# Kernel tuning notes

Measured on AMD Instinct MI355X. Metric: run time of the kernel, lower is better.

## Reference

```python
import jax, jax.numpy as jnp
import numpy as np

RES = 128          # image / k-space resolution
DECIMATION = 4     # acceleration factor
P = RES * RES // DECIMATION  # 4096 trajectory points
B = 8              # batch


def setup_inputs() -> dict:
    key = jax.random.key(0)
    k1, k2 = jax.random.split(key)
    k_space_input = jax.random.normal(k1, (B, 1, RES, RES, 2), dtype=jnp.float32)
    # learnable k-space trajectory in pixel units, range [-RES/2, RES/2]
    trajectory = (jax.random.uniform(k2, (P, 2), dtype=jnp.float32) - 0.5) * RES
    return {"k_space_input": k_space_input, "trajectory": trajectory}


def _grid_sample_points(img, pts_norm):
    """torch.nn.functional.grid_sample (bilinear, zero padding, align_corners=False)
    evaluated at a list of points.
    img: (B, C, H, W); pts_norm: (P, 2) in [-1, 1], [:, 0] -> x (W axis), [:, 1] -> y (H axis).
    Returns (B, C, P)."""
    H, W = img.shape[-2], img.shape[-1]
    x = (pts_norm[:, 0] + 1.0) * (W * 0.5) - 0.5
    y = (pts_norm[:, 1] + 1.0) * (H * 0.5) - 0.5
    x0f = jnp.floor(x)
    y0f = jnp.floor(y)
    wx = x - x0f  # differentiable interpolation weights
    wy = y - y0f
    x0 = x0f.astype(jnp.int32)
    y0 = y0f.astype(jnp.int32)

    def tap(ix, iy, w):
        valid = ((ix >= 0) & (ix < W) & (iy >= 0) & (iy < H)).astype(img.dtype)
        ixc = jnp.clip(ix, 0, W - 1)
        iyc = jnp.clip(iy, 0, H - 1)
        return img[:, :, iyc, ixc] * (w * valid)  # (B, C, P)

    return (tap(x0, y0, (1 - wx) * (1 - wy))
            + tap(x0 + 1, y0, wx * (1 - wy))
            + tap(x0, y0 + 1, (1 - wx) * wy)
            + tap(x0 + 1, y0 + 1, wx * wy))


def _forward(k_space_input, trajectory):
    # (B,1,H,W,2) -> (B,2,H,W): channels = (real, imag)
    ksp = jnp.transpose(k_space_input, (0, 1, 4, 2, 3))[:, 0]
    # bilinear resampling of cartesian k-space at the trajectory points
    pts = trajectory / (RES * 0.5)  # normalize to [-1, 1] as in the torch helper
    sub = _grid_sample_points(ksp, pts)            # (B, 2, P)
    c = sub[:, 0] + 1j * sub[:, 1]                 # complex measurements (B, P)
    # adjoint (type-1) NUFFT back to a centered RES x RES image grid:
    # img[y, x] = (1/RES) * sum_p c[p] * exp(+2*pi*i*(ky_p*y + kx_p*x)/RES)
    xs = jnp.arange(RES, dtype=jnp.float32) - RES * 0.5  # centered grid coords
    phase = (2.0 * jnp.pi / RES)
    Ax = jnp.exp(1j * phase * trajectory[:, 0][:, None] * xs[None, :])  # (P, W)
    Ay = jnp.exp(1j * phase * trajectory[:, 1][:, None] * xs[None, :])  # (P, H)
    tmp = c[:, :, None] * Ay[None, :, :]           # (B, P, H)
    img = jnp.einsum('bph,pw->bhw', tmp, Ax) / RES  # (B, H, W), 1/sqrt(H*W) scale
    out = jnp.stack([img.real, img.imag], axis=-1)[:, None]  # (B, 1, H, W, 2)
    return out


def reference(k_space_input, trajectory):
    return _forward(k_space_input, trajectory)
```

## Files before the change

kernel.cpp:

```cpp
#include <hip/hip_runtime.h>

#define RES    128
#define P_PTS  4096
#define CHUNKS 16
#define PP     256

typedef _Float16 half8  __attribute__((ext_vector_type(8)));
typedef _Float16 half2v __attribute__((ext_vector_type(2)));
typedef float    f32x4  __attribute__((ext_vector_type(4)));

__global__ __launch_bounds__(256) void gemm_kernel(const float* __restrict__ ksp,
                                                   const float* __restrict__ traj,
                                                   half2v* __restrict__ part) {
    __shared__ float2 st[PP];
    __shared__ float2 sc[PP];
    __shared__ __align__(16) _Float16 sA[4096];
    __shared__ __align__(16) _Float16 sB[8192];

    const int chunk = blockIdx.x;
    const int b     = blockIdx.y >> 1;
    const int mh    = blockIdx.y & 1;
    const int tid   = threadIdx.x;
    const int wave  = tid >> 6;
    const int lane  = tid & 63;
    const int l15   = lane & 15;
    const int q     = lane >> 4;

    {
        const int p = chunk * PP + tid;
        const float tx = traj[2 * p], ty = traj[2 * p + 1];
        st[tid] = make_float2(tx, ty);
        const float x = tx + 63.5f, y = ty + 63.5f;
        const float x0f = floorf(x), y0f = floorf(y);
        const float wx = x - x0f, wy = y - y0f;
        const int ix0 = (int)x0f, iy0 = (int)y0f;
        float re = 0.0f, im = 0.0f;
#pragma unroll
        for (int dy = 0; dy < 2; ++dy) {
#pragma unroll
            for (int dx = 0; dx < 2; ++dx) {
                const int ix = ix0 + dx, iy = iy0 + dy;
                const float w = (dx ? wx : 1.0f - wx) * (dy ? wy : 1.0f - wy);
                if (ix >= 0 && ix < RES && iy >= 0 && iy < RES) {
                    const float2 v = *(const float2*)(ksp + ((b * RES + iy) * RES + ix) * 2);
                    re = fmaf(v.x, w, re);
                    im = fmaf(v.y, w, im);
                }
            }
        }
        sc[tid] = make_float2(re * (1.0f / 128.0f), im * (1.0f / 128.0f));
    }
    __syncthreads();

    f32x4 accR[4][2], accI[4][2];
#pragma unroll
    for (int i = 0; i < 4; ++i)
#pragma unroll
        for (int j = 0; j < 2; ++j) {
            accR[i][j] = (f32x4){0.f, 0.f, 0.f, 0.f};
            accI[i][j] = (f32x4){0.f, 0.f, 0.f, 0.f};
        }

    const float inv = 1.0f / 128.0f;
    const int nB = tid & 127, kB = tid >> 7;
    const int mA = tid & 63,  kA = tid >> 6;
    const float xn = ((float)nB - 64.0f) * inv;
    const float xm = ((float)(mh * 64 + mA) - 64.0f) * inv;

    for (int r = 0; r < 8; ++r) {
        const int p0 = r * 32;
#pragma unroll
        for (int i = 0; i < 4; ++i) {
            const int k8l = kB + 2 * i;
            half8 v;
#pragma unroll
            for (int j = 0; j < 4; ++j) {
                const int pl = p0 + k8l * 4 + j;
                const float rev = st[pl].x * xn;
                const float f = rev - floorf(rev);
                v[2 * j]     = (_Float16)__builtin_amdgcn_cosf(f);
                v[2 * j + 1] = (_Float16)__builtin_amdgcn_sinf(f);
            }
            *(half8*)(sB + ((size_t)(k8l * 128 + nB)) * 8) = v;
        }
#pragma unroll
        for (int i = 0; i < 2; ++i) {
            const int k8l = kA + 4 * i;
            half8 v;
#pragma unroll
            for (int j = 0; j < 4; ++j) {
                const int pl = p0 + k8l * 4 + j;
                const float rev = st[pl].y * xm;
                const float f = rev - floorf(rev);
                const float cs = __builtin_amdgcn_cosf(f);
                const float sn = __builtin_amdgcn_sinf(f);
                const float cr = sc[pl].x, ci = sc[pl].y;
                v[2 * j]     = (_Float16)(cr * cs - ci * sn);
                v[2 * j + 1] = (_Float16)(cr * sn + ci * cs);
            }
            *(half8*)(sA + ((size_t)(k8l * 64 + mA)) * 8) = v;
        }
        __syncthreads();

#pragma unroll
        for (int s = 0; s < 2; ++s) {
            const _Float16* pa = sA + (s * 4 + q) * 512;
            const _Float16* pb = sB + (s * 4 + q) * 1024;
            half8 an[4], bv[2], a1[4], a2[4];
#pragma unroll
            for (int mt = 0; mt < 4; ++mt)
                an[mt] = *(const half8*)(pa + (mt * 16 + l15) * 8);
#pragma unroll
            for (int nt = 0; nt < 2; ++nt)
                bv[nt] = *(const half8*)(pb + (wave * 32 + nt * 16 + l15) * 8);
            const half8 SGN = {(_Float16)1.f, (_Float16)-1.f, (_Float16)1.f, (_Float16)-1.f,
                               (_Float16)1.f, (_Float16)-1.f, (_Float16)1.f, (_Float16)-1.f};
#pragma unroll
            for (int mt = 0; mt < 4; ++mt) {
                a1[mt] = an[mt] * SGN;
                a2[mt] = __builtin_shufflevector(an[mt], an[mt],
                                                 1, 0, 3, 2, 5, 4, 7, 6);
            }
#pragma unroll
            for (int mt = 0; mt < 4; ++mt)
#pragma unroll
                for (int nt = 0; nt < 2; ++nt) {
                    accR[mt][nt] = __builtin_amdgcn_mfma_f32_16x16x32_f16(
                        a1[mt], bv[nt], accR[mt][nt], 0, 0, 0);
                    accI[mt][nt] = __builtin_amdgcn_mfma_f32_16x16x32_f16(
                        a2[mt], bv[nt], accI[mt][nt], 0, 0, 0);
                }
        }
        __syncthreads();
    }

#pragma unroll
    for (int mt = 0; mt < 4; ++mt) {
#pragma unroll
        for (int nt = 0; nt < 2; ++nt) {
            const int n = wave * 32 + nt * 16 + l15;
#pragma unroll
            for (int rg = 0; rg < 4; ++rg) {
                const int m = b * 128 + mh * 64 + mt * 16 + q * 4 + rg;
                half2v pv;
                pv[0] = (_Float16)accR[mt][nt][rg];
                pv[1] = (_Float16)accI[mt][nt][rg];
                part[(size_t)chunk * 131072 + m * 128 + n] = pv;
            }
        }
    }
}

__global__ __launch_bounds__(256) void reduce_kernel(const half2v* __restrict__ part,
                                                     float2* __restrict__ out) {
    const int i = blockIdx.x * 256 + threadIdx.x;
    float sr = 0.f, si = 0.f;
#pragma unroll
    for (int c = 0; c < CHUNKS; ++c) {
        half2v v = part[(size_t)c * 131072 + i];
        sr += (float)v[0];
        si += (float)v[1];
    }
    out[i] = make_float2(sr, si);
}

extern "C" void kernel_launch(void* const* d_in, const int* in_sizes, int n_in,
                              void* d_out, int out_size, void* d_ws, size_t ws_size,
                              hipStream_t stream) {
    const float* ksp  = (const float*)d_in[0];
    const float* traj = (const float*)d_in[1];
    half2v* part = (half2v*)d_ws;

    hipLaunchKernelGGL(gemm_kernel,   dim3(CHUNKS, 16), dim3(256), 0, stream,
                       ksp, traj, part);
    hipLaunchKernelGGL(reduce_kernel, dim3(512),        dim3(256), 0, stream,
                       part, (float2*)d_out);
}
```

Measured before the change: 74.01 us.

## Precompute twiddle operands in a prep kernel and stream them into MFMA GEMM

Moves the sin/cos twiddle generation and the complex-weighted Ay operand out of the GEMM kernel into a separate prep kernel that writes fp16 operand tables to workspace. Previously every block recomputed these per batch and half-tile. The GEMM now loads operands straight from global memory with no LDS and no barriers, splits N across a third grid dimension, and moves the sign and swap onto the B operand. The reduce kernel is vectorized to half8 loads. The cost is an extra launch plus a global-memory round trip for the operand tables.

```diff
diff --git a/kernel.cpp b/kernel.cpp
--- a/kernel.cpp
+++ b/kernel.cpp
@@ -3,94 +3,75 @@
 #define RES    128
 #define P_PTS  4096
 #define CHUNKS 16
-#define PP     256
 
 typedef _Float16 half8  __attribute__((ext_vector_type(8)));
 typedef _Float16 half2v __attribute__((ext_vector_type(2)));
 typedef float    f32x4  __attribute__((ext_vector_type(4)));
 
-__global__ __launch_bounds__(256) void gemm_kernel(const float* __restrict__ ksp,
+#define AX_OFF   8388608
+#define AYC_OFF 10485760
+
+__global__ __launch_bounds__(256) void prep_kernel(const float* __restrict__ ksp,
                                                    const float* __restrict__ traj,
-                                                   half2v* __restrict__ part) {
-    __shared__ float2 st[PP];
-    __shared__ float2 sc[PP];
-    __shared__ __align__(16) _Float16 sA[4096];
-    __shared__ __align__(16) _Float16 sB[8192];
+                                                   half8* __restrict__ Ax_t,
+                                                   half8* __restrict__ Ayc_t) {
+    __shared__ float2 st[128];
+    __shared__ float2 sc[128];
+    const int gc  = blockIdx.x;
+    const int bb  = blockIdx.y;
+    const int tid = threadIdx.x;
 
-    const int chunk = blockIdx.x;
-    const int b     = blockIdx.y >> 1;
-    const int mh    = blockIdx.y & 1;
-    const int tid   = threadIdx.x;
-    const int wave  = tid >> 6;
-    const int lane  = tid & 63;
-    const int l15   = lane & 15;
-    const int q     = lane >> 4;
-
-    {
-        const int p = chunk * PP + tid;
+    if (tid < 128) {
+        const int p = gc * 128 + tid;
         const float tx = traj[2 * p], ty = traj[2 * p + 1];
         st[tid] = make_float2(tx, ty);
-        const float x = tx + 63.5f, y = ty + 63.5f;
-        const float x0f = floorf(x), y0f = floorf(y);
-        const float wx = x - x0f, wy = y - y0f;
-        const int ix0 = (int)x0f, iy0 = (int)y0f;
-        float re = 0.0f, im = 0.0f;
+        if (bb < 8) {
+            const float x = tx + 63.5f, y = ty + 63.5f;
+            const float x0f = floorf(x), y0f = floorf(y);
+            const float wx = x - x0f, wy = y - y0f;
+            const int ix0 = (int)x0f, iy0 = (int)y0f;
+            float re = 0.0f, im = 0.0f;
 #pragma unroll
-        for (int dy = 0; dy < 2; ++dy) {
+            for (int dy = 0; dy < 2; ++dy) {
 #pragma unroll
-            for (int dx = 0; dx < 2; ++dx) {
-                const int ix = ix0 + dx, iy = iy0 + dy;
-                const float w = (dx ? wx : 1.0f - wx) * (dy ? wy : 1.0f - wy);
-                if (ix >= 0 && ix < RES && iy >= 0 && iy < RES) {
-                    const float2 v = *(const float2*)(ksp + ((b * RES + iy) * RES + ix) * 2);
-                    re = fmaf(v.x, w, re);
-                    im = fmaf(v.y, w, im);
+                for (int dx = 0; dx < 2; ++dx) {
+                    const int ix = ix0 + dx, iy = iy0 + dy;
+                    const float w = (dx ? wx : 1.0f - wx) * (dy ? wy : 1.0f - wy);
+                    if (ix >= 0 && ix < RES && iy >= 0 && iy < RES) {
+                        const float2 v = *(const float2*)(ksp + ((bb * RES + iy) * RES + ix) * 2);
+                        re = fmaf(v.x, w, re);
+                        im = fmaf(v.y, w, im);
+                    }
                 }
             }
+            sc[tid] = make_float2(re * (1.0f / 128.0f), im * (1.0f / 128.0f));
         }
-        sc[tid] = make_float2(re * (1.0f / 128.0f), im * (1.0f / 128.0f));
     }
     __syncthreads();
 
-    f32x4 accR[4][2], accI[4][2];
+    const float inv = 1.0f / 128.0f;
 #pragma unroll
-    for (int i = 0; i < 4; ++i)
-#pragma unroll
-        for (int j = 0; j < 2; ++j) {
-            accR[i][j] = (f32x4){0.f, 0.f, 0.f, 0.f};
-            accI[i][j] = (f32x4){0.f, 0.f, 0.f, 0.f};
-        }
-
-    const float inv = 1.0f / 128.0f;
-    const int nB = tid & 127, kB = tid >> 7;
-    const int mA = tid & 63,  kA = tid >> 6;
-    const float xn = ((float)nB - 64.0f) * inv;
-    const float xm = ((float)(mh * 64 + mA) - 64.0f) * inv;
-
-    for (int r = 0; r < 8; ++r) {
-        const int p0 = r * 32;
-#pragma unroll
-        for (int i = 0; i < 4; ++i) {
-            const int k8l = kB + 2 * i;
-            half8 v;
+    for (int k = 0; k < 16; ++k) {
+        const int e   = k * 256 + tid;
+        const int gl  = e >> 7;
+        const int col = e & 127;
+        const float xc = ((float)col - 64.0f) * inv;
+        half8 v;
+        if (bb == 8) {
 #pragma unroll
             for (int j = 0; j < 4; ++j) {
-                const int pl = p0 + k8l * 4 + j;
-                const float rev = st[pl].x * xn;
+                const int pl = gl * 4 + j;
+                const float rev = st[pl].x * xc;
                 const float f = rev - floorf(rev);
                 v[2 * j]     = (_Float16)__builtin_amdgcn_cosf(f);
                 v[2 * j + 1] = (_Float16)__builtin_amdgcn_sinf(f);
             }
-            *(half8*)(sB + ((size_t)(k8l * 128 + nB)) * 8) = v;
-        }
-#pragma unroll
-        for (int i = 0; i < 2; ++i) {
-            const int k8l = kA + 4 * i;
-            half8 v;
+            Ax_t[(size_t)(gc * 32 + gl) * 128 + col] = v;
+        } else {
 #pragma unroll
             for (int j = 0; j < 4; ++j) {
-                const int pl = p0 + k8l * 4 + j;
-                const float rev = st[pl].y * xm;
+                const int pl = gl * 4 + j;
+                const float rev = st[pl].y * xc;
                 const float f = rev - floorf(rev);
                 const float cs = __builtin_amdgcn_cosf(f);
                 const float sn = __builtin_amdgcn_sinf(f);
@@ -98,70 +79,84 @@
                 v[2 * j]     = (_Float16)(cr * cs - ci * sn);
                 v[2 * j + 1] = (_Float16)(cr * sn + ci * cs);
             }
-            *(half8*)(sA + ((size_t)(k8l * 64 + mA)) * 8) = v;
+            Ayc_t[((size_t)bb * 1024 + gc * 32 + gl) * 128 + col] = v;
         }
-        __syncthreads();
+    }
+}
 
+__global__ __launch_bounds__(256, 2) void gemm_kernel(const half8* __restrict__ Ax_t,
+                                                      const half8* __restrict__ Ayc_t,
+                                                      half2v* __restrict__ part) {
+    const int chunk = blockIdx.x;
+    const int b     = blockIdx.y >> 1;
+    const int mh    = blockIdx.y & 1;
+    const int nh    = blockIdx.z;
+    const int tid   = threadIdx.x;
+    const int wave  = tid >> 6;
+    const int lane  = tid & 63;
+    const int l15   = lane & 15;
+    const int q     = lane >> 4;
+
+    const int ncol = nh * 64 + wave * 16 + l15;
+    const half8* bp = Ax_t  + (size_t)(chunk * 64 + q) * 128 + ncol;
+    const half8* ap = Ayc_t + ((size_t)b * 1024 + chunk * 64 + q) * 128 + mh * 64 + l15;
+
+    f32x4 accR[4], accI[4];
 #pragma unroll
-        for (int s = 0; s < 2; ++s) {
-            const _Float16* pa = sA + (s * 4 + q) * 512;
-            const _Float16* pb = sB + (s * 4 + q) * 1024;
-            half8 an[4], bv[2], a1[4], a2[4];
+    for (int i = 0; i < 4; ++i) {
+        accR[i] = (f32x4){0.f, 0.f, 0.f, 0.f};
+        accI[i] = (f32x4){0.f, 0.f, 0.f, 0.f};
+    }
+
+    const half8 SGN = {(_Float16)1.f, (_Float16)-1.f, (_Float16)1.f, (_Float16)-1.f,
+                       (_Float16)1.f, (_Float16)-1.f, (_Float16)1.f, (_Float16)-1.f};
+
+#pragma unroll 4
+    for (int ks = 0; ks < 16; ++ks) {
+        const half8 bv = bp[(size_t)ks * 512];
+        const half8 b1 = bv * SGN;
+        const half8 b2 = __builtin_shufflevector(bv, bv,
+                                                 1, 0, 3, 2, 5, 4, 7, 6);
+        half8 an[4];
 #pragma unroll
-            for (int mt = 0; mt < 4; ++mt)
-                an[mt] = *(const half8*)(pa + (mt * 16 + l15) * 8);
+        for (int mt = 0; mt < 4; ++mt)
+            an[mt] = ap[(size_t)ks * 512 + mt * 16];
 #pragma unroll
-            for (int nt = 0; nt < 2; ++nt)
-                bv[nt] = *(const half8*)(pb + (wave * 32 + nt * 16 + l15) * 8);
-            const half8 SGN = {(_Float16)1.f, (_Float16)-1.f, (_Float16)1.f, (_Float16)-1.f,
-                               (_Float16)1.f, (_Float16)-1.f, (_Float16)1.f, (_Float16)-1.f};
-#pragma unroll
-            for (int mt = 0; mt < 4; ++mt) {
-                a1[mt] = an[mt] * SGN;
-                a2[mt] = __builtin_shufflevector(an[mt], an[mt],
-                                                 1, 0, 3, 2, 5, 4, 7, 6);
-            }
-#pragma unroll
-            for (int mt = 0; mt < 4; ++mt)
-#pragma unroll
-                for (int nt = 0; nt < 2; ++nt) {
-                    accR[mt][nt] = __builtin_amdgcn_mfma_f32_16x16x32_f16(
-                        a1[mt], bv[nt], accR[mt][nt], 0, 0, 0);
-                    accI[mt][nt] = __builtin_amdgcn_mfma_f32_16x16x32_f16(
-                        a2[mt], bv[nt], accI[mt][nt], 0, 0, 0);
-                }
+        for (int mt = 0; mt < 4; ++mt) {
+            accR[mt] = __builtin_amdgcn_mfma_f32_16x16x32_f16(an[mt], b1, accR[mt], 0, 0, 0);
+            accI[mt] = __builtin_amdgcn_mfma_f32_16x16x32_f16(an[mt], b2, accI[mt], 0, 0, 0);
         }
-        __syncthreads();
     }
 
 #pragma unroll
     for (int mt = 0; mt < 4; ++mt) {
 #pragma unroll
-        for (int nt = 0; nt < 2; ++nt) {
-            const int n = wave * 32 + nt * 16 + l15;
-#pragma unroll
-            for (int rg = 0; rg < 4; ++rg) {
-                const int m = b * 128 + mh * 64 + mt * 16 + q * 4 + rg;
-                half2v pv;
-                pv[0] = (_Float16)accR[mt][nt][rg];
-                pv[1] = (_Float16)accI[mt][nt][rg];
-                part[(size_t)chunk * 131072 + m * 128 + n] = pv;
-            }
+        for (int rg = 0; rg < 4; ++rg) {
+            const int m = b * 128 + mh * 64 + mt * 16 + q * 4 + rg;
+            half2v pv;
+            pv[0] = (_Float16)accR[mt][rg];
+            pv[1] = (_Float16)accI[mt][rg];
+            part[(size_t)chunk * 131072 + m * 128 + ncol] = pv;
         }
     }
 }
 
-__global__ __launch_bounds__(256) void reduce_kernel(const half2v* __restrict__ part,
-                                                     float2* __restrict__ out) {
+__global__ __launch_bounds__(256) void reduce_kernel(const half8* __restrict__ part,
+                                                     f32x4* __restrict__ out) {
     const int i = blockIdx.x * 256 + threadIdx.x;
-    float sr = 0.f, si = 0.f;
+    float s[8];
+#pragma unroll
+    for (int k = 0; k < 8; ++k) s[k] = 0.f;
 #pragma unroll
     for (int c = 0; c < CHUNKS; ++c) {
-        half2v v = part[(size_t)c * 131072 + i];
-        sr += (float)v[0];
-        si += (float)v[1];
+        const half8 v = part[(size_t)c * 32768 + i];
+#pragma unroll
+        for (int k = 0; k < 8; ++k) s[k] += (float)v[k];
     }
-    out[i] = make_float2(sr, si);
+    f32x4 lo = {s[0], s[1], s[2], s[3]};
+    f32x4 hi = {s[4], s[5], s[6], s[7]};
+    out[2 * i]     = lo;
+    out[2 * i + 1] = hi;
 }
 
 extern "C" void kernel_launch(void* const* d_in, const int* in_sizes, int n_in,
@@ -170,9 +165,13 @@
     const float* ksp  = (const float*)d_in[0];
     const float* traj = (const float*)d_in[1];
     half2v* part = (half2v*)d_ws;
+    half8*  Ax   = (half8*)((char*)d_ws + AX_OFF);
+    half8*  Ayc  = (half8*)((char*)d_ws + AYC_OFF);
 
-    hipLaunchKernelGGL(gemm_kernel,   dim3(CHUNKS, 16), dim3(256), 0, stream,
-                       ksp, traj, part);
-    hipLaunchKernelGGL(reduce_kernel, dim3(512),        dim3(256), 0, stream,
-                       part, (float2*)d_out);
+    hipLaunchKernelGGL(prep_kernel,   dim3(32, 9),     dim3(256), 0, stream,
+                       ksp, traj, Ax, Ayc);
+    hipLaunchKernelGGL(gemm_kernel,   dim3(CHUNKS, 16, 2), dim3(256), 0, stream,
+                       Ax, Ayc, part);
+    hipLaunchKernelGGL(reduce_kernel, dim3(128),       dim3(256), 0, stream,
+                       (const half8*)d_ws, (f32x4*)d_out);
 }
```

After: 89.71 us. +21.2%, slower.

## Double chunk count, apply complex sign/swap on B, vectorize reduction loads

Applied to the files above, without the earlier changes.

Splits the trajectory into 32 chunks of 128 points instead of 16 of 256, doubling the gemm grid to 512 blocks so more CUs are busy. The sign flip and real/imag swap for the complex product move from the four A fragments to the two B fragments, cutting per-step vector work. The reduction reads 8 halfs per thread and launches fewer threads. The cost is twice as many partial-result writes and reads through the workspace, and half the block's threads sit idle during the gather stage.

```diff
diff --git a/kernel.cpp b/kernel.cpp
--- a/kernel.cpp
+++ b/kernel.cpp
@@ -2,8 +2,8 @@
 
 #define RES    128
 #define P_PTS  4096
-#define CHUNKS 16
-#define PP     256
+#define CHUNKS 32
+#define PP     128
 
 typedef _Float16 half8  __attribute__((ext_vector_type(8)));
 typedef _Float16 half2v __attribute__((ext_vector_type(2)));
@@ -26,7 +26,7 @@
     const int l15   = lane & 15;
     const int q     = lane >> 4;
 
-    {
+    if (tid < PP) {
         const int p = chunk * PP + tid;
         const float tx = traj[2 * p], ty = traj[2 * p + 1];
         st[tid] = make_float2(tx, ty);
@@ -67,7 +67,7 @@
     const float xn = ((float)nB - 64.0f) * inv;
     const float xm = ((float)(mh * 64 + mA) - 64.0f) * inv;
 
-    for (int r = 0; r < 8; ++r) {
+    for (int r = 0; r < 4; ++r) {
         const int p0 = r * 32;
 #pragma unroll
         for (int i = 0; i < 4; ++i) {
@@ -102,23 +102,21 @@
         }
         __syncthreads();
 
+        const half8 SGN = {(_Float16)1.f, (_Float16)-1.f, (_Float16)1.f, (_Float16)-1.f,
+                           (_Float16)1.f, (_Float16)-1.f, (_Float16)1.f, (_Float16)-1.f};
 #pragma unroll
         for (int s = 0; s < 2; ++s) {
             const _Float16* pa = sA + (s * 4 + q) * 512;
             const _Float16* pb = sB + (s * 4 + q) * 1024;
-            half8 an[4], bv[2], a1[4], a2[4];
+            half8 an[4], b1[2], b2[2];
 #pragma unroll
             for (int mt = 0; mt < 4; ++mt)
                 an[mt] = *(const half8*)(pa + (mt * 16 + l15) * 8);
 #pragma unroll
-            for (int nt = 0; nt < 2; ++nt)
-                bv[nt] = *(const half8*)(pb + (wave * 32 + nt * 16 + l15) * 8);
-            const half8 SGN = {(_Float16)1.f, (_Float16)-1.f, (_Float16)1.f, (_Float16)-1.f,
-                               (_Float16)1.f, (_Float16)-1.f, (_Float16)1.f, (_Float16)-1.f};
-#pragma unroll
-            for (int mt = 0; mt < 4; ++mt) {
-                a1[mt] = an[mt] * SGN;
-                a2[mt] = __builtin_shufflevector(an[mt], an[mt],
+            for (int nt = 0; nt < 2; ++nt) {
+                const half8 bv = *(const half8*)(pb + (wave * 32 + nt * 16 + l15) * 8);
+                b1[nt] = bv * SGN;
+                b2[nt] = __builtin_shufflevector(bv, bv,
                                                  1, 0, 3, 2, 5, 4, 7, 6);
             }
 #pragma unroll
@@ -126,9 +124,9 @@
 #pragma unroll
                 for (int nt = 0; nt < 2; ++nt) {
                     accR[mt][nt] = __builtin_amdgcn_mfma_f32_16x16x32_f16(
-                        a1[mt], bv[nt], accR[mt][nt], 0, 0, 0);
+                        an[mt], b1[nt], accR[mt][nt], 0, 0, 0);
                     accI[mt][nt] = __builtin_amdgcn_mfma_f32_16x16x32_f16(
-                        a2[mt], bv[nt], accI[mt][nt], 0, 0, 0);
+                        an[mt], b2[nt], accI[mt][nt], 0, 0, 0);
                 }
         }
         __syncthreads();
@@ -151,17 +149,22 @@
     }
 }
 
-__global__ __launch_bounds__(256) void reduce_kernel(const half2v* __restrict__ part,
-                                                     float2* __restrict__ out) {
+__global__ __launch_bounds__(256) void reduce_kernel(const half8* __restrict__ part,
+                                                     f32x4* __restrict__ out) {
     const int i = blockIdx.x * 256 + threadIdx.x;
-    float sr = 0.f, si = 0.f;
+    float s[8];
+#pragma unroll
+    for (int k = 0; k < 8; ++k) s[k] = 0.f;
 #pragma unroll
     for (int c = 0; c < CHUNKS; ++c) {
-        half2v v = part[(size_t)c * 131072 + i];
-        sr += (float)v[0];
-        si += (float)v[1];
+        const half8 v = part[(size_t)c * 32768 + i];
+#pragma unroll
+        for (int k = 0; k < 8; ++k) s[k] += (float)v[k];
     }
-    out[i] = make_float2(sr, si);
+    f32x4 lo = {s[0], s[1], s[2], s[3]};
+    f32x4 hi = {s[4], s[5], s[6], s[7]};
+    out[2 * i]     = lo;
+    out[2 * i + 1] = hi;
 }
 
 extern "C" void kernel_launch(void* const* d_in, const int* in_sizes, int n_in,
@@ -173,6 +176,6 @@
 
     hipLaunchKernelGGL(gemm_kernel,   dim3(CHUNKS, 16), dim3(256), 0, stream,
                        ksp, traj, part);
-    hipLaunchKernelGGL(reduce_kernel, dim3(512),        dim3(256), 0, stream,
-                       part, (float2*)d_out);
+    hipLaunchKernelGGL(reduce_kernel, dim3(128),        dim3(256), 0, stream,
+                       (const half8*)part, (f32x4*)d_out);
 }
```

Measured after the change: 74.98 us. No clear change (+1.3%).

## Fuse GEMM and reduction into one kernel with in-block split-K over all points

Applied to the files above, without the earlier changes.

Replaces the chunked two-kernel scheme (per-chunk partial outputs written to workspace in fp16, then reduced by a second kernel) with a single kernel. Each block owns a 32x16 output tile and loops over all 4096 points, with 8 waves splitting K and reducing through shared memory. Twiddle factors are generated directly in registers with no LDS staging, and a precomputed 16-row phase shift derives the second M-tile from the first to save sin/cos work. The cost is that every block recomputes the bilinear sampling for all points, and uses large LDS, which limits occupancy.

```diff
diff --git a/kernel.cpp b/kernel.cpp
--- a/kernel.cpp
+++ b/kernel.cpp
@@ -1,167 +1,124 @@
 #include <hip/hip_runtime.h>
 
-#define RES    128
-#define P_PTS  4096
-#define CHUNKS 16
-#define PP     256
+#define RES 128
 
-typedef _Float16 half8  __attribute__((ext_vector_type(8)));
-typedef _Float16 half2v __attribute__((ext_vector_type(2)));
-typedef float    f32x4  __attribute__((ext_vector_type(4)));
+typedef _Float16 half8 __attribute__((ext_vector_type(8)));
+typedef float    f32x4 __attribute__((ext_vector_type(4)));
 
-__global__ __launch_bounds__(256) void gemm_kernel(const float* __restrict__ ksp,
-                                                   const float* __restrict__ traj,
-                                                   half2v* __restrict__ part) {
-    __shared__ float2 st[PP];
-    __shared__ float2 sc[PP];
-    __shared__ __align__(16) _Float16 sA[4096];
-    __shared__ __align__(16) _Float16 sB[8192];
+__global__ __launch_bounds__(512, 2) void fused_kernel(const float* __restrict__ ksp,
+                                                       const float* __restrict__ traj,
+                                                       float2* __restrict__ out) {
+    __shared__ float2 st[4096];
+    __shared__ float2 sc[4096];
+    __shared__ float2 sd[4096];
+    __shared__ float  red[8192];
 
-    const int chunk = blockIdx.x;
-    const int b     = blockIdx.y >> 1;
-    const int mh    = blockIdx.y & 1;
-    const int tid   = threadIdx.x;
-    const int wave  = tid >> 6;
-    const int lane  = tid & 63;
-    const int l15   = lane & 15;
-    const int q     = lane >> 4;
+    const int bid  = blockIdx.x;
+    const int b    = bid >> 5;
+    const int mt   = (bid >> 3) & 3;
+    const int nt   = bid & 7;
+    const int m0   = mt * 32, n0 = nt * 16;
+    const int tid  = threadIdx.x;
+    const int w    = tid >> 6;
+    const int lane = tid & 63;
+    const int l15  = lane & 15;
+    const int q    = lane >> 4;
 
-    {
-        const int p = chunk * PP + tid;
-        const float tx = traj[2 * p], ty = traj[2 * p + 1];
-        st[tid] = make_float2(tx, ty);
-        const float x = tx + 63.5f, y = ty + 63.5f;
+#pragma unroll
+    for (int it = 0; it < 8; ++it) {
+        const int p = it * 512 + tid;
+        const float2 t2 = *(const float2*)(traj + 2 * p);
+        st[p] = t2;
+        const float x = t2.x + 63.5f, y = t2.y + 63.5f;
         const float x0f = floorf(x), y0f = floorf(y);
         const float wx = x - x0f, wy = y - y0f;
         const int ix0 = (int)x0f, iy0 = (int)y0f;
-        float re = 0.0f, im = 0.0f;
+        float re = 0.f, im = 0.f;
 #pragma unroll
-        for (int dy = 0; dy < 2; ++dy) {
+        for (int dy = 0; dy < 2; ++dy)
 #pragma unroll
             for (int dx = 0; dx < 2; ++dx) {
                 const int ix = ix0 + dx, iy = iy0 + dy;
-                const float w = (dx ? wx : 1.0f - wx) * (dy ? wy : 1.0f - wy);
+                const float wgt = (dx ? wx : 1.f - wx) * (dy ? wy : 1.f - wy);
                 if (ix >= 0 && ix < RES && iy >= 0 && iy < RES) {
                     const float2 v = *(const float2*)(ksp + ((b * RES + iy) * RES + ix) * 2);
-                    re = fmaf(v.x, w, re);
-                    im = fmaf(v.y, w, im);
+                    re = fmaf(v.x, wgt, re);
+                    im = fmaf(v.y, wgt, im);
                 }
             }
-        }
-        sc[tid] = make_float2(re * (1.0f / 128.0f), im * (1.0f / 128.0f));
+        sc[p] = make_float2(re * (1.f / 128.f), im * (1.f / 128.f));
+        const float rd = t2.y * 0.125f;
+        const float fd = rd - floorf(rd);
+        sd[p] = make_float2(__builtin_amdgcn_cosf(fd), __builtin_amdgcn_sinf(fd));
     }
     __syncthreads();
 
-    f32x4 accR[4][2], accI[4][2];
+    f32x4 accR0 = {0.f, 0.f, 0.f, 0.f};
+    f32x4 accI0 = {0.f, 0.f, 0.f, 0.f};
+    f32x4 accR1 = {0.f, 0.f, 0.f, 0.f};
+    f32x4 accI1 = {0.f, 0.f, 0.f, 0.f};
+
+    const float inv = 1.f / 128.f;
+    const float xm = ((float)(m0 + l15) - 64.f) * inv;
+    const float xn = ((float)(n0 + l15) - 64.f) * inv;
+    const half8 SGN = {(_Float16)1.f, (_Float16)-1.f, (_Float16)1.f, (_Float16)-1.f,
+                       (_Float16)1.f, (_Float16)-1.f, (_Float16)1.f, (_Float16)-1.f};
+    const int pw = w * 512 + q * 4;
+
+    for (int s = 0; s < 32; ++s) {
+        half8 av0, av1, bv;
 #pragma unroll
-    for (int i = 0; i < 4; ++i)
-#pragma unroll
-        for (int j = 0; j < 2; ++j) {
-            accR[i][j] = (f32x4){0.f, 0.f, 0.f, 0.f};
-            accI[i][j] = (f32x4){0.f, 0.f, 0.f, 0.f};
+        for (int j = 0; j < 4; ++j) {
+            const int p = pw + s * 16 + j;
+            const float2 t2 = st[p];
+            const float2 c2 = sc[p];
+            const float2 d2 = sd[p];
+            float rb = t2.x * xn;
+            rb -= floorf(rb);
+            bv[2 * j]     = (_Float16)__builtin_amdgcn_cosf(rb);
+            bv[2 * j + 1] = (_Float16)__builtin_amdgcn_sinf(rb);
+            float ra = t2.y * xm;
+            ra -= floorf(ra);
+            const float cs = __builtin_amdgcn_cosf(ra);
+            const float sn = __builtin_amdgcn_sinf(ra);
+            const float ar0 = c2.x * cs - c2.y * sn;
+            const float ai0 = c2.x * sn + c2.y * cs;
+            av0[2 * j]     = (_Float16)ar0;
+            av0[2 * j + 1] = (_Float16)ai0;
+            av1[2 * j]     = (_Float16)(ar0 * d2.x - ai0 * d2.y);
+            av1[2 * j + 1] = (_Float16)(ar0 * d2.y + ai0 * d2.x);
         }
-
-    const float inv = 1.0f / 128.0f;
-    const int nB = tid & 127, kB = tid >> 7;
-    const int mA = tid & 63,  kA = tid >> 6;
-    const float xn = ((float)nB - 64.0f) * inv;
-    const float xm = ((float)(mh * 64 + mA) - 64.0f) * inv;
-
-    for (int r = 0; r < 8; ++r) {
-        const int p0 = r * 32;
-#pragma unroll
-        for (int i = 0; i < 4; ++i) {
-            const int k8l = kB + 2 * i;
-            half8 v;
-#pragma unroll
-            for (int j = 0; j < 4; ++j) {
-                const int pl = p0 + k8l * 4 + j;
-                const float rev = st[pl].x * xn;
-                const float f = rev - floorf(rev);
-                v[2 * j]     = (_Float16)__builtin_amdgcn_cosf(f);
-                v[2 * j + 1] = (_Float16)__builtin_amdgcn_sinf(f);
-            }
-            *(half8*)(sB + ((size_t)(k8l * 128 + nB)) * 8) = v;
-        }
-#pragma unroll
-        for (int i = 0; i < 2; ++i) {
-            const int k8l = kA + 4 * i;
-            half8 v;
-#pragma unroll
-            for (int j = 0; j < 4; ++j) {
-                const int pl = p0 + k8l * 4 + j;
-                const float rev = st[pl].y * xm;
-                const float f = rev - floorf(rev);
-                const float cs = __builtin_amdgcn_cosf(f);
-                const float sn = __builtin_amdgcn_sinf(f);
-                const float cr = sc[pl].x, ci = sc[pl].y;
-                v[2 * j]     = (_Float16)(cr * cs - ci * sn);
-                v[2 * j + 1] = (_Float16)(cr * sn + ci * cs);
-            }
-            *(half8*)(sA + ((size_t)(k8l * 64 + mA)) * 8) = v;
-        }
-        __syncthreads();
-
-#pragma unroll
-        for (int s = 0; s < 2; ++s) {
-            const _Float16* pa = sA + (s * 4 + q) * 512;
-            const _Float16* pb = sB + (s * 4 + q) * 1024;
-            half8 an[4], bv[2], a1[4], a2[4];
-#pragma unroll
-            for (int mt = 0; mt < 4; ++mt)
-                an[mt] = *(const half8*)(pa + (mt * 16 + l15) * 8);
-#pragma unroll
-            for (int nt = 0; nt < 2; ++nt)
-                bv[nt] = *(const half8*)(pb + (wave * 32 + nt * 16 + l15) * 8);
-            const half8 SGN = {(_Float16)1.f, (_Float16)-1.f, (_Float16)1.f, (_Float16)-1.f,
-                               (_Float16)1.f, (_Float16)-1.f, (_Float16)1.f, (_Float16)-1.f};
-#pragma unroll
-            for (int mt = 0; mt < 4; ++mt) {
-                a1[mt] = an[mt] * SGN;
-                a2[mt] = __builtin_shufflevector(an[mt], an[mt],
+        const half8 b1 = bv * SGN;
+        const half8 b2 = __builtin_shufflevector(bv, bv,
                                                  1, 0, 3, 2, 5, 4, 7, 6);
-            }
-#pragma unroll
-            for (int mt = 0; mt < 4; ++mt)
-#pragma unroll
-                for (int nt = 0; nt < 2; ++nt) {
-                    accR[mt][nt] = __builtin_amdgcn_mfma_f32_16x16x32_f16(
-                        a1[mt], bv[nt], accR[mt][nt], 0, 0, 0);
-                    accI[mt][nt] = __builtin_amdgcn_mfma_f32_16x16x32_f16(
-                        a2[mt], bv[nt], accI[mt][nt], 0, 0, 0);
-                }
-        }
-        __syncthreads();
+        accR0 = __builtin_amdgcn_mfma_f32_16x16x32_f16(av0, b1, accR0, 0, 0, 0);
+        accI0 = __builtin_amdgcn_mfma_f32_16x16x32_f16(av0, b2, accI0, 0, 0, 0);
+        accR1 = __builtin_amdgcn_mfma_f32_16x16x32_f16(av1, b1, accR1, 0, 0, 0);
+        accI1 = __builtin_amdgcn_mfma_f32_16x16x32_f16(av1, b2, accI1, 0, 0, 0);
     }
 
+    float* rw = red + w * 1024;
 #pragma unroll
-    for (int mt = 0; mt < 4; ++mt) {
-#pragma unroll
-        for (int nt = 0; nt < 2; ++nt) {
-            const int n = wave * 32 + nt * 16 + l15;
-#pragma unroll
-            for (int rg = 0; rg < 4; ++rg) {
-                const int m = b * 128 + mh * 64 + mt * 16 + q * 4 + rg;
-                half2v pv;
-                pv[0] = (_Float16)accR[mt][nt][rg];
-                pv[1] = (_Float16)accI[mt][nt][rg];
-                part[(size_t)chunk * 131072 + m * 128 + n] = pv;
-            }
-        }
+    for (int rg = 0; rg < 4; ++rg) {
+        const int r0 = ((q * 4 + rg) * 16 + l15) * 2;
+        rw[r0]     = accR0[rg];
+        rw[r0 + 1] = accI0[rg];
+        const int r1 = ((16 + q * 4 + rg) * 16 + l15) * 2;
+        rw[r1]     = accR1[rg];
+        rw[r1 + 1] = accI1[rg];
     }
-}
+    __syncthreads();
 
-__global__ __launch_bounds__(256) void reduce_kernel(const half2v* __restrict__ part,
-                                                     float2* __restrict__ out) {
-    const int i = blockIdx.x * 256 + threadIdx.x;
+    const int lm = tid >> 4;
+    const int ln = tid & 15;
+    const int ri = (lm * 16 + ln) * 2;
     float sr = 0.f, si = 0.f;
 #pragma unroll
-    for (int c = 0; c < CHUNKS; ++c) {
-        half2v v = part[(size_t)c * 131072 + i];
-        sr += (float)v[0];
-        si += (float)v[1];
+    for (int ww = 0; ww < 8; ++ww) {
+        sr += red[ww * 1024 + ri];
+        si += red[ww * 1024 + ri + 1];
     }
-    out[i] = make_float2(sr, si);
+    out[(b * RES + m0 + lm) * RES + n0 + ln] = make_float2(sr, si);
 }
 
 extern "C" void kernel_launch(void* const* d_in, const int* in_sizes, int n_in,
@@ -169,10 +126,7 @@
                               hipStream_t stream) {
     const float* ksp  = (const float*)d_in[0];
     const float* traj = (const float*)d_in[1];
-    half2v* part = (half2v*)d_ws;
 
-    hipLaunchKernelGGL(gemm_kernel,   dim3(CHUNKS, 16), dim3(256), 0, stream,
-                       ksp, traj, part);
-    hipLaunchKernelGGL(reduce_kernel, dim3(512),        dim3(256), 0, stream,
-                       part, (float2*)d_out);
+    hipLaunchKernelGGL(fused_kernel, dim3(256), dim3(512), 0, stream,
+                       ksp, traj, (float2*)d_out);
 }
```

New measurement: 84.15 us. +13.7%, slower.
